# Performance work log

Hardware: AMD Instinct MI355X
Metric: run time of the kernel (lower is better)

Reference implementation:

```python
import jax, jax.numpy as jnp
import numpy as np

N = 100000   # nodes
E = 1200000  # edges
G = 512      # graphs in batch
H = 64       # hidden_dim
EED = 8      # edge_emb_dim
VOCABS = (120, 10, 7, 5, 2)
EDIMS = (64, 16, 8, 8, 4)
BN_EPS = 1e-5


def _lin(x, w, b):
    # torch nn.Linear: y = x @ W^T + b
    return x @ w.T + b


def setup_inputs() -> dict:
    key = jax.random.key(0)
    ks = iter(jax.random.split(key, 64))
    s = 0.02
    d = {}
    d["x"] = jax.random.randint(next(ks), (N, 5), 0, 120)
    d["edge_index"] = jax.random.randint(next(ks), (2, E), 0, N)
    d["edge_attr"] = jax.random.randint(next(ks), (E, 3), 0, 16)
    d["batch"] = jnp.sort(jax.random.randint(next(ks), (N,), 0, G))
    for i, (v, dd) in enumerate(zip(VOCABS, EDIMS)):
        d[f"emb{i}"] = jax.random.normal(next(ks), (v, dd), jnp.float32) * s
    d["proj_w"] = jax.random.normal(next(ks), (H, sum(EDIMS)), jnp.float32) * s
    d["proj_b"] = jnp.zeros((H,), jnp.float32)
    for i in (1, 2, 3):
        d[f"eemb{i}"] = jax.random.normal(next(ks), (16, EED), jnp.float32) * s
        d[f"lin_e{i}_w"] = jax.random.normal(next(ks), (H, EED), jnp.float32) * s
        d[f"lin_e{i}_b"] = jnp.zeros((H,), jnp.float32)
        d[f"eps{i}"] = jnp.zeros((), jnp.float32)
        d[f"mlp{i}_w1"] = jax.random.normal(next(ks), (H, H), jnp.float32) * s
        d[f"mlp{i}_b1"] = jnp.zeros((H,), jnp.float32)
        d[f"mlp{i}_w2"] = jax.random.normal(next(ks), (H, H), jnp.float32) * s
        d[f"mlp{i}_b2"] = jnp.zeros((H,), jnp.float32)
    d["bn_g"] = jnp.ones((H,), jnp.float32)
    d["bn_b"] = jnp.zeros((H,), jnp.float32)
    d["bn_rm"] = jnp.zeros((H,), jnp.float32)
    d["bn_rv"] = jnp.ones((H,), jnp.float32)
    d["gate_w"] = jax.random.normal(next(ks), (1, H), jnp.float32) * s
    d["gate_b"] = jnp.zeros((1,), jnp.float32)
    d["head_w1"] = jax.random.normal(next(ks), (128, H), jnp.float32) * s
    d["head_b1"] = jnp.zeros((128,), jnp.float32)
    d["head_w2"] = jax.random.normal(next(ks), (1, 128), jnp.float32) * s
    d["head_b2"] = jnp.zeros((1,), jnp.float32)
    return d


def reference(x, edge_index, edge_attr, batch,
              emb0, emb1, emb2, emb3, emb4, proj_w, proj_b,
              eemb1, lin_e1_w, lin_e1_b, eps1, mlp1_w1, mlp1_b1, mlp1_w2, mlp1_b2,
              eemb2, lin_e2_w, lin_e2_b, eps2, mlp2_w1, mlp2_b1, mlp2_w2, mlp2_b2,
              eemb3, lin_e3_w, lin_e3_b, eps3, mlp3_w1, mlp3_b1, mlp3_w2, mlp3_b2,
              bn_g, bn_b, bn_rm, bn_rv, gate_w, gate_b,
              head_w1, head_b1, head_w2, head_b2):
    # --- node embedding lookup (clamped per-table, as in torch) ---
    tabs = [emb0, emb1, emb2, emb3, emb4]
    feats = [t[jnp.clip(x[:, i], 0, t.shape[0] - 1)] for i, t in enumerate(tabs)]
    h = jnp.concatenate(feats, axis=-1)            # [N, 100]
    h = _lin(h, proj_w, proj_b)                    # [N, H]  (dropout = identity, eval)

    # --- edge hash, shared by all blocks ---
    eh = (edge_attr[:, 0] + 3 * edge_attr[:, 1] + 7 * edge_attr[:, 2]) % 16  # [E]
    src, dst = edge_index[0], edge_index[1]

    def gine(h, eemb, lw, lb, eps, w1, b1, w2, b2):
        # GINEConv: mlp((1+eps) x_i + sum_j relu(x_j + lin(e_ij)))
        e = _lin(eemb[eh], lw, lb)                        # [E, H]
        msg = jax.nn.relu(h[src] + e)                     # [E, H] gather + combine
        agg = jax.ops.segment_sum(msg, dst, num_segments=N)  # scatter-add to targets
        z = (1.0 + eps) * h + agg
        return _lin(jax.nn.relu(_lin(z, w1, b1)), w2, b2)

    h = jax.nn.relu(gine(h, eemb1, lin_e1_w, lin_e1_b, eps1, mlp1_w1, mlp1_b1, mlp1_w2, mlp1_b2))
    h = jax.nn.relu(gine(h, eemb2, lin_e2_w, lin_e2_b, eps2, mlp2_w1, mlp2_b1, mlp2_w2, mlp2_b2))
    h = jax.nn.relu(gine(h, eemb3, lin_e3_w, lin_e3_b, eps3, mlp3_w1, mlp3_b1, mlp3_w2, mlp3_b2))

    # BatchNorm1d (eval mode, running stats)
    h = (h - bn_rm) * jax.lax.rsqrt(bn_rv + BN_EPS) * bn_g + bn_b

    # AttentionalAggregation: segment softmax over gate, weighted segment sum
    gate = _lin(h, gate_w, gate_b)[:, 0]                  # [N]
    m = jax.ops.segment_max(gate, batch, num_segments=G)  # [G]
    w = jnp.exp(gate - m[batch])
    den = jax.ops.segment_sum(w, batch, num_segments=G) + 1e-16
    alpha = w / den[batch]                                # [N]
    graph = jax.ops.segment_sum(alpha[:, None] * h, batch, num_segments=G)  # [G, H]

    out = _lin(jax.nn.relu(_lin(graph, head_w1, head_b1)), head_w2, head_b2)  # [G, 1]
    return out[:, 0]
```

## Files before the change

kernel.cpp:

```cpp
#include <hip/hip_runtime.h>
#include <stdint.h>

#define N_NODES 100000
#define N_EDGES 1200000
#define N_GRAPH 512
#define HID 64

#define NBUCK 391
#define BCAP  4096
#define CHUNK 4096

#define PRE_W0  (144 * 64 + 3 * 1024 + 64 + NBUCK)
#define PRE_JOBS (PRE_W0 + 6 * 4096)

typedef __attribute__((ext_vector_type(8))) short bshort8;
typedef __attribute__((ext_vector_type(4))) float f32x4;

__device__ __forceinline__ unsigned short f2bf(float f) {
    unsigned u = __float_as_uint(f);
    u += 0x7FFF + ((u >> 16) & 1);
    return (unsigned short)(u >> 16);
}
__device__ __forceinline__ float bf2f(unsigned short b) {
    return __uint_as_float((unsigned)b << 16);
}

__global__ __launch_bounds__(256) void k_pre(
    const float* emb0, const float* emb1, const float* emb2, const float* emb3, const float* emb4,
    const float* proj_w,
    const float* ee1, const float* lw1, const float* lb1,
    const float* ee2, const float* lw2, const float* lb2,
    const float* ee3, const float* lw3, const float* lb3,
    const float* bn_g, const float* bn_b, const float* bn_rm, const float* bn_rv,
    const float* w11, const float* w12, const float* w21, const float* w22,
    const float* w31, const float* w32,
    float* ptab, float* elin, float* bnsc, float* bnsh, int* cursor,
    unsigned short* wbf)
{
    int job = blockIdx.x * 256 + threadIdx.x;
    if (job < 144 * 64) {
        int row = job >> 6, c = job & 63;
        const float* emb; int lr, dim, off;
        if (row < 120)      { emb = emb0; lr = row;       dim = 64; off = 0;  }
        else if (row < 130) { emb = emb1; lr = row - 120; dim = 16; off = 64; }
        else if (row < 137) { emb = emb2; lr = row - 130; dim = 8;  off = 80; }
        else if (row < 142) { emb = emb3; lr = row - 137; dim = 8;  off = 88; }
        else                { emb = emb4; lr = row - 142; dim = 4;  off = 96; }
        float s = 0.f;
        for (int d = 0; d < dim; ++d)
            s += emb[lr * dim + d] * proj_w[c * 100 + off + d];
        ptab[row * 64 + c] = s;
    } else if (job < 144 * 64 + 3 * 1024) {
        int j = job - 144 * 64;
        int L = j >> 10; int r = (j >> 6) & 15; int c = j & 63;
        const float* ee = (L == 0) ? ee1 : (L == 1) ? ee2 : ee3;
        const float* lw = (L == 0) ? lw1 : (L == 1) ? lw2 : lw3;
        const float* lb = (L == 0) ? lb1 : (L == 1) ? lb2 : lb3;
        float s = lb[c];
        for (int d = 0; d < 8; ++d) s += ee[r * 8 + d] * lw[c * 8 + d];
        elin[j] = s;
    } else if (job < 144 * 64 + 3 * 1024 + 64) {
        int c = job - (144 * 64 + 3 * 1024);
        float sc = bn_g[c] * rsqrtf(bn_rv[c] + 1e-5f);
        bnsc[c] = sc;
        bnsh[c] = bn_b[c] - bn_rm[c] * sc;
    } else if (job < PRE_W0) {
        cursor[job - (144 * 64 + 3 * 1024 + 64)] = 0;
    } else if (job < PRE_JOBS) {
        int j2 = job - PRE_W0;
        int sel = j2 >> 12;
        const float* W = (sel == 0) ? w11 : (sel == 1) ? w12 : (sel == 2) ? w21
                       : (sel == 3) ? w22 : (sel == 4) ? w31 : w32;
        wbf[j2] = f2bf(W[j2 & 4095]);
    }
}

__global__ __launch_bounds__(256) void k_embed(const int* x, const float* ptab,
                                               const float* proj_b, float* h,
                                               unsigned short* h2) {
    int id = blockIdx.x * 256 + threadIdx.x;
    if (id >= N_NODES * HID) return;
    int n = id >> 6, c = id & 63;
    const int* xr = x + n * 5;
    int r0 = min(max(xr[0], 0), 119);
    int r1 = 120 + min(max(xr[1], 0), 9);
    int r2 = 130 + min(max(xr[2], 0), 6);
    int r3 = 137 + min(max(xr[3], 0), 4);
    int r4 = 142 + min(max(xr[4], 0), 1);
    float v = proj_b[c] + ptab[r0 * 64 + c] + ptab[r1 * 64 + c] + ptab[r2 * 64 + c]
            + ptab[r3 * 64 + c] + ptab[r4 * 64 + c];
    h[id] = v;
    h2[id] = f2bf(v);
}

__global__ __launch_bounds__(256) void k_gptr(const int* batch, int* gptr) {
    int n = blockIdx.x * 256 + threadIdx.x;
    if (n >= N_NODES) return;
    int b = batch[n];
    int bp = (n == 0) ? -1 : batch[n - 1];
    for (int g = bp + 1; g <= b; ++g) gptr[g] = n;
    if (n == N_NODES - 1) {
        for (int g = b + 1; g <= N_GRAPH; ++g) gptr[g] = N_NODES;
    }
}

__global__ __launch_bounds__(256) void k_bin(const int* __restrict__ ei,
                                             const int* __restrict__ ea,
                                             int* __restrict__ cursor,
                                             int* __restrict__ binned) {
    __shared__ int pay[CHUNK];
    __shared__ unsigned short bkid[CHUNK];
    __shared__ int hist[NBUCK], inc[NBUCK], tmp[NBUCK], gdelta[NBUCK];
    int t = threadIdx.x;
    int e0 = blockIdx.x * CHUNK;
    for (int i = t; i < NBUCK; i += 256) hist[i] = 0;
    __syncthreads();
    int mypay[16], myrb[16];
    #pragma unroll
    for (int j = 0; j < 16; ++j) {
        int e = e0 + j * 256 + t;
        myrb[j] = -1;
        if (e < N_EDGES) {
            int s = ei[e];
            int d = ei[N_EDGES + e];
            int hsh = (ea[e * 3] + 3 * ea[e * 3 + 1] + 7 * ea[e * 3 + 2]) & 15;
            int b = d >> 8;
            mypay[j] = s | (hsh << 17) | ((d & 255) << 21);
            int r = atomicAdd(&hist[b], 1);
            myrb[j] = r | (b << 12);
        }
    }
    __syncthreads();
    for (int i = t; i < NBUCK; i += 256) inc[i] = hist[i];
    __syncthreads();
    for (int off = 1; off < NBUCK; off <<= 1) {
        for (int i = t; i < NBUCK; i += 256) tmp[i] = inc[i] + ((i >= off) ? inc[i - off] : 0);
        __syncthreads();
        for (int i = t; i < NBUCK; i += 256) inc[i] = tmp[i];
        __syncthreads();
    }
    for (int i = t; i < NBUCK; i += 256) {
        int c = hist[i];
        int gp = c ? atomicAdd(&cursor[i], c) : 0;
        gdelta[i] = i * BCAP + gp - (inc[i] - c);
    }
    __syncthreads();
    #pragma unroll
    for (int j = 0; j < 16; ++j) {
        if (myrb[j] >= 0) {
            int b = myrb[j] >> 12, r = myrb[j] & 0xFFF;
            int slot = (inc[b] - hist[b]) + r;
            pay[slot] = mypay[j];
            bkid[slot] = (unsigned short)b;
        }
    }
    __syncthreads();
    int tot = inc[NBUCK - 1];
    for (int i = t; i < tot; i += 256)
        binned[gdelta[bkid[i]] + i] = pay[i];
}

__global__ __launch_bounds__(512) void k_bscan(const int* cursor, int* bbase, int* rowptr) {
    __shared__ int s[512], tp[512];
    int t = threadIdx.x;
    int v = (t < NBUCK) ? cursor[t] : 0;
    s[t] = v;
    __syncthreads();
    for (int off = 1; off < 512; off <<= 1) {
        tp[t] = s[t] + ((t >= off) ? s[t - off] : 0);
        __syncthreads();
        s[t] = tp[t];
        __syncthreads();
    }
    if (t < NBUCK) bbase[t] = s[t] - v;
    if (t == 0) { bbase[NBUCK] = N_EDGES; rowptr[N_NODES] = N_EDGES; }
}

__global__ __launch_bounds__(256) void k_fin(const int* __restrict__ binned,
                                             const int* __restrict__ cursor,
                                             const int* __restrict__ bbase,
                                             int* __restrict__ rowptr,
                                             int* __restrict__ epk) {
    __shared__ int h2[256], sc[256], cur[256];
    int b = blockIdx.x, t = threadIdx.x;
    int cnt = cursor[b];
    int gb = bbase[b];
    int node0 = b << 8;
    h2[t] = 0;
    __syncthreads();
    const int* bp = binned + b * BCAP;
    for (int i = t; i < cnt; i += 256) atomicAdd(&h2[(bp[i] >> 21) & 255], 1);
    __syncthreads();
    sc[t] = h2[t];
    __syncthreads();
    for (int off = 1; off < 256; off <<= 1) {
        int v = (t >= off) ? sc[t - off] : 0;
        __syncthreads();
        sc[t] += v;
        __syncthreads();
    }
    int ex = sc[t] - h2[t];
    cur[t] = ex;
    int n = node0 + t;
    if (n < N_NODES) rowptr[n] = gb + ex;
    __syncthreads();
    for (int i = t; i < cnt; i += 256) {
        int p = bp[i];
        int pos = atomicAdd(&cur[(p >> 21) & 255], 1);
        epk[gb + pos] = p & 0x1FFFFF;
    }
}

__global__ __launch_bounds__(256) void k_gather(const unsigned short* __restrict__ h2,
                                                const float* __restrict__ elinL,
                                                const int* __restrict__ rowptr,
                                                const int* __restrict__ epk,
                                                float* __restrict__ agg) {
    __shared__ float es[16 * 64];
    int t = threadIdx.x;
    ((float4*)es)[t] = ((const float4*)elinL)[t];
    __syncthreads();
    int n = blockIdx.x * 4 + (t >> 6);
    if (n >= N_NODES) return;
    int lane = t & 63;
    int grp = lane >> 4;
    int c4 = (lane & 15) << 2;
    int p0 = rowptr[n], p1 = rowptr[n + 1];
    float4 acc = make_float4(0.f, 0.f, 0.f, 0.f);
    int p = p0 + grp;
    while (p + 4 < p1) {
        int pk0 = epk[p];
        int pk1 = epk[p + 4];
        ushort4 a0 = *(const ushort4*)(h2 + (pk0 & 0x1FFFF) * 64 + c4);
        ushort4 a1 = *(const ushort4*)(h2 + (pk1 & 0x1FFFF) * 64 + c4);
        float4 e0 = *(const float4*)(es + ((pk0 >> 17) & 15) * 64 + c4);
        float4 e1 = *(const float4*)(es + ((pk1 >> 17) & 15) * 64 + c4);
        acc.x += fmaxf(bf2f(a0.x) + e0.x, 0.f) + fmaxf(bf2f(a1.x) + e1.x, 0.f);
        acc.y += fmaxf(bf2f(a0.y) + e0.y, 0.f) + fmaxf(bf2f(a1.y) + e1.y, 0.f);
        acc.z += fmaxf(bf2f(a0.z) + e0.z, 0.f) + fmaxf(bf2f(a1.z) + e1.z, 0.f);
        acc.w += fmaxf(bf2f(a0.w) + e0.w, 0.f) + fmaxf(bf2f(a1.w) + e1.w, 0.f);
        p += 8;
    }
    if (p < p1) {
        int pk0 = epk[p];
        ushort4 a0 = *(const ushort4*)(h2 + (pk0 & 0x1FFFF) * 64 + c4);
        float4 e0 = *(const float4*)(es + ((pk0 >> 17) & 15) * 64 + c4);
        acc.x += fmaxf(bf2f(a0.x) + e0.x, 0.f);
        acc.y += fmaxf(bf2f(a0.y) + e0.y, 0.f);
        acc.z += fmaxf(bf2f(a0.z) + e0.z, 0.f);
        acc.w += fmaxf(bf2f(a0.w) + e0.w, 0.f);
    }
    acc.x += __shfl_down(acc.x, 32, 64);
    acc.y += __shfl_down(acc.y, 32, 64);
    acc.z += __shfl_down(acc.z, 32, 64);
    acc.w += __shfl_down(acc.w, 32, 64);
    acc.x += __shfl_down(acc.x, 16, 64);
    acc.y += __shfl_down(acc.y, 16, 64);
    acc.z += __shfl_down(acc.z, 16, 64);
    acc.w += __shfl_down(acc.w, 16, 64);
    if (grp == 0) *(float4*)(agg + n * 64 + c4) = acc;
}

__global__ __launch_bounds__(256) void k_mlpm(const float* __restrict__ hin,
                                              const float* __restrict__ agg,
                                              const float* __restrict__ epsp,
                                              const unsigned short* __restrict__ wbf1,
                                              const float* __restrict__ b1,
                                              const unsigned short* __restrict__ wbf2,
                                              const float* __restrict__ b2,
                                              float* __restrict__ out,
                                              unsigned short* __restrict__ h2out,
                                              const float* __restrict__ bnsc,
                                              const float* __restrict__ bnsh,
                                              const float* __restrict__ gate_w,
                                              const float* __restrict__ gate_b,
                                              float* __restrict__ gate) {
    __shared__ unsigned short zb[64 * 72];
    __shared__ unsigned short hb[64 * 72];
    int t = threadIdx.x;
    int row0 = blockIdx.x * 64;
    float epsv = 1.f + epsp[0];
    for (int idx = t; idx < 1024; idx += 256) {
        int r = idx >> 4, c4 = (idx & 15) << 2;
        int gr = row0 + r;
        float4 v = make_float4(0.f, 0.f, 0.f, 0.f);
        if (gr < N_NODES) {
            float4 a = *(const float4*)(hin + gr * 64 + c4);
            float4 b = *(const float4*)(agg + gr * 64 + c4);
            v.x = epsv * a.x + b.x; v.y = epsv * a.y + b.y;
            v.z = epsv * a.z + b.z; v.w = epsv * a.w + b.w;
        }
        ushort4 zv;
        zv.x = f2bf(v.x); zv.y = f2bf(v.y); zv.z = f2bf(v.z); zv.w = f2bf(v.w);
        *(ushort4*)(zb + r * 72 + c4) = zv;
    }
    int lane = t & 63, wv = t >> 6;
    int quad = lane >> 4, lc = lane & 15;
    int m0 = wv * 16;
    bshort8 w1f[4][2];
    #pragma unroll
    for (int nt = 0; nt < 4; ++nt)
        #pragma unroll
        for (int kt = 0; kt < 2; ++kt)
            w1f[nt][kt] = *(const bshort8*)(wbf1 + (nt * 16 + lc) * 64 + kt * 32 + quad * 8);
    bshort8 w2f[4][2];
    #pragma unroll
    for (int nt = 0; nt < 4; ++nt)
        #pragma unroll
        for (int kt = 0; kt < 2; ++kt)
            w2f[nt][kt] = *(const bshort8*)(wbf2 + (nt * 16 + lc) * 64 + kt * 32 + quad * 8);
    __syncthreads();
    bshort8 a0 = *(const bshort8*)(zb + (m0 + lc) * 72 + quad * 8);
    bshort8 a1 = *(const bshort8*)(zb + (m0 + lc) * 72 + 32 + quad * 8);
    f32x4 acc1[4];
    #pragma unroll
    for (int nt = 0; nt < 4; ++nt) {
        acc1[nt] = (f32x4){0.f, 0.f, 0.f, 0.f};
        acc1[nt] = __builtin_amdgcn_mfma_f32_16x16x32_bf16(a0, w1f[nt][0], acc1[nt], 0, 0, 0);
        acc1[nt] = __builtin_amdgcn_mfma_f32_16x16x32_bf16(a1, w1f[nt][1], acc1[nt], 0, 0, 0);
    }
    #pragma unroll
    for (int nt = 0; nt < 4; ++nt) {
        float bb = b1[nt * 16 + lc];
        #pragma unroll
        for (int reg = 0; reg < 4; ++reg) {
            float v = fmaxf(acc1[nt][reg] + bb, 0.f);
            hb[(m0 + quad * 4 + reg) * 72 + nt * 16 + lc] = f2bf(v);
        }
    }
    bshort8 c0 = *(const bshort8*)(hb + (m0 + lc) * 72 + quad * 8);
    bshort8 c1 = *(const bshort8*)(hb + (m0 + lc) * 72 + 32 + quad * 8);
    f32x4 acc2[4];
    #pragma unroll
    for (int nt = 0; nt < 4; ++nt) {
        acc2[nt] = (f32x4){0.f, 0.f, 0.f, 0.f};
        acc2[nt] = __builtin_amdgcn_mfma_f32_16x16x32_bf16(c0, w2f[nt][0], acc2[nt], 0, 0, 0);
        acc2[nt] = __builtin_amdgcn_mfma_f32_16x16x32_bf16(c1, w2f[nt][1], acc2[nt], 0, 0, 0);
    }
    if (gate == nullptr) {
        #pragma unroll
        for (int reg = 0; reg < 4; ++reg) {
            int gr = row0 + m0 + quad * 4 + reg;
            if (gr < N_NODES) {
                #pragma unroll
                for (int nt = 0; nt < 4; ++nt) {
                    int col = nt * 16 + lc;
                    float v = fmaxf(acc2[nt][reg] + b2[col], 0.f);
                    out[gr * 64 + col] = v;
                    h2out[gr * 64 + col] = f2bf(v);
                }
            }
        }
    } else {
        float gb = gate_b[0];
        #pragma unroll
        for (int reg = 0; reg < 4; ++reg) {
            int gr = row0 + m0 + quad * 4 + reg;
            float p = 0.f;
            #pragma unroll
            for (int nt = 0; nt < 4; ++nt) {
                int col = nt * 16 + lc;
                float v = fmaxf(acc2[nt][reg] + b2[col], 0.f) * bnsc[col] + bnsh[col];
                p += v * gate_w[col];
                if (gr < N_NODES) out[gr * 64 + col] = v;
            }
            p += __shfl_down(p, 8, 16);
            p += __shfl_down(p, 4, 16);
            p += __shfl_down(p, 2, 16);
            p += __shfl_down(p, 1, 16);
            if (lc == 0 && gr < N_NODES) gate[gr] = p + gb;
        }
    }
}

__global__ __launch_bounds__(256) void k_att(const float* __restrict__ h,
                                             const float* __restrict__ gate,
                                             const int* __restrict__ gptr,
                                             const float* __restrict__ hw1,
                                             const float* __restrict__ hb1,
                                             const float* __restrict__ hw2,
                                             const float* __restrict__ hb2,
                                             float* __restrict__ out) {
    __shared__ float red[4];
    __shared__ float acc_s[4][64];
    __shared__ float gvec[64];
    __shared__ float m_s, den_s;
    int t = threadIdx.x, g = blockIdx.x;
    int n0 = gptr[g], n1 = gptr[g + 1];
    float m = -INFINITY;
    for (int n = n0 + t; n < n1; n += 256) m = fmaxf(m, gate[n]);
    #pragma unroll
    for (int off = 32; off > 0; off >>= 1) m = fmaxf(m, __shfl_down(m, off, 64));
    if ((t & 63) == 0) red[t >> 6] = m;
    __syncthreads();
    if (t == 0) m_s = fmaxf(fmaxf(red[0], red[1]), fmaxf(red[2], red[3]));
    __syncthreads();
    m = m_s;
    float s = 0.f;
    for (int n = n0 + t; n < n1; n += 256) s += expf(gate[n] - m);
    #pragma unroll
    for (int off = 32; off > 0; off >>= 1) s += __shfl_down(s, off, 64);
    if ((t & 63) == 0) red[t >> 6] = s;
    __syncthreads();
    if (t == 0) den_s = red[0] + red[1] + red[2] + red[3] + 1e-16f;
    __syncthreads();
    float invden = 1.f / den_s;
    int c = t & 63, w = t >> 6;
    float acc = 0.f;
    for (int n = n0 + w; n < n1; n += 4) {
        float a = expf(gate[n] - m);
        acc += a * h[n * 64 + c];
    }
    acc_s[w][c] = acc;
    __syncthreads();
    if (w == 0)
        gvec[c] = (acc_s[0][c] + acc_s[1][c] + acc_s[2][c] + acc_s[3][c]) * invden;
    __syncthreads();
    float p = 0.f;
    if (t < 128) {
        float sh = hb1[t];
        const float* wr = hw1 + t * 64;
        #pragma unroll
        for (int k = 0; k < 64; ++k) sh += gvec[k] * wr[k];
        p = fmaxf(sh, 0.f) * hw2[t];
    }
    #pragma unroll
    for (int off = 32; off > 0; off >>= 1) p += __shfl_down(p, off, 64);
    if (t == 0) red[0] = p;
    if (t == 64) red[1] = p;
    __syncthreads();
    if (t == 0) out[g] = red[0] + red[1] + hb2[0];
}

extern "C" void kernel_launch(void* const* d_in, const int* in_sizes, int n_in,
                              void* d_out, int out_size, void* d_ws, size_t ws_size,
                              hipStream_t stream) {
    const int* x    = (const int*)d_in[0];
    const int* ei   = (const int*)d_in[1];
    const int* ea   = (const int*)d_in[2];
    const int* bat  = (const int*)d_in[3];
    const float* emb0 = (const float*)d_in[4];
    const float* emb1 = (const float*)d_in[5];
    const float* emb2 = (const float*)d_in[6];
    const float* emb3 = (const float*)d_in[7];
    const float* emb4 = (const float*)d_in[8];
    const float* proj_w = (const float*)d_in[9];
    const float* proj_b = (const float*)d_in[10];
    const float* bn_g  = (const float*)d_in[35];
    const float* bn_b  = (const float*)d_in[36];
    const float* bn_rm = (const float*)d_in[37];
    const float* bn_rv = (const float*)d_in[38];
    const float* gate_w = (const float*)d_in[39];
    const float* gate_b = (const float*)d_in[40];
    const float* head_w1 = (const float*)d_in[41];
    const float* head_b1 = (const float*)d_in[42];
    const float* head_w2 = (const float*)d_in[43];
    const float* head_b2 = (const float*)d_in[44];

    char* wsb = (char*)d_ws;
    size_t o = 0;
    auto alloc = [&](size_t bytes) -> void* {
        void* p = wsb + o;
        o += (bytes + 255) & ~(size_t)255;
        return p;
    };
    float* ptab   = (float*)alloc(144 * 64 * 4);
    float* elin   = (float*)alloc(3 * 16 * 64 * 4);
    float* bnsc   = (float*)alloc(64 * 4);
    float* bnsh   = (float*)alloc(64 * 4);
    int* cursor   = (int*)alloc(NBUCK * 4);
    int* bbase    = (int*)alloc((NBUCK + 1) * 4);
    int* gptr     = (int*)alloc((N_GRAPH + 1) * 4);
    int* rowptr   = (int*)alloc(((size_t)N_NODES + 1) * 4);
    int* binned   = (int*)alloc((size_t)NBUCK * BCAP * 4);
    int* epk      = (int*)alloc((size_t)N_EDGES * 4);
    float* h      = (float*)alloc((size_t)N_NODES * 64 * 4);
    unsigned short* h2 = (unsigned short*)alloc((size_t)N_NODES * 64 * 2);
    float* agg    = (float*)alloc((size_t)N_NODES * 64 * 4);
    float* gate   = (float*)alloc((size_t)N_NODES * 4);
    unsigned short* wbf = (unsigned short*)alloc(6 * 4096 * 2);

    k_pre<<<(PRE_JOBS + 255) / 256, 256, 0, stream>>>(
                                  emb0, emb1, emb2, emb3, emb4, proj_w,
                                  (const float*)d_in[11], (const float*)d_in[12], (const float*)d_in[13],
                                  (const float*)d_in[19], (const float*)d_in[20], (const float*)d_in[21],
                                  (const float*)d_in[27], (const float*)d_in[28], (const float*)d_in[29],
                                  bn_g, bn_b, bn_rm, bn_rv,
                                  (const float*)d_in[15], (const float*)d_in[17],
                                  (const float*)d_in[23], (const float*)d_in[25],
                                  (const float*)d_in[31], (const float*)d_in[33],
                                  ptab, elin, bnsc, bnsh, cursor, wbf);
    k_embed<<<(N_NODES * 64 + 255) / 256, 256, 0, stream>>>(x, ptab, proj_b, h, h2);
    k_gptr<<<(N_NODES + 255) / 256, 256, 0, stream>>>(bat, gptr);
    k_bin<<<(N_EDGES + CHUNK - 1) / CHUNK, 256, 0, stream>>>(ei, ea, cursor, binned);
    k_bscan<<<1, 512, 0, stream>>>(cursor, bbase, rowptr);
    k_fin<<<NBUCK, 256, 0, stream>>>(binned, cursor, bbase, rowptr, epk);

    for (int L = 0; L < 3; ++L) {
        const float* epsp = (const float*)d_in[14 + L * 8];
        const float* b1   = (const float*)d_in[16 + L * 8];
        const float* b2   = (const float*)d_in[18 + L * 8];
        const unsigned short* wb1 = wbf + (L * 2 + 0) * 4096;
        const unsigned short* wb2 = wbf + (L * 2 + 1) * 4096;
        k_gather<<<(N_NODES + 3) / 4, 256, 0, stream>>>(h2, elin + L * 1024, rowptr, epk, agg);
        if (L < 2) {
            k_mlpm<<<(N_NODES + 63) / 64, 256, 0, stream>>>(h, agg, epsp, wb1, b1, wb2, b2, h, h2,
                                                            nullptr, nullptr, nullptr, nullptr,
                                                            nullptr);
        } else {
            k_mlpm<<<(N_NODES + 63) / 64, 256, 0, stream>>>(h, agg, epsp, wb1, b1, wb2, b2, h, nullptr,
                                                            bnsc, bnsh, gate_w, gate_b, gate);
        }
    }

    k_att<<<N_GRAPH, 256, 0, stream>>>(h, gate, gptr, head_w1, head_b1, head_w2, head_b2,
                                       (float*)d_out);
}
```

Measured before the change: 445.3 us.

## Drop fp32 node features, keep bf16 only; preload edge indices via shuffle

Removes the fp32 copy of node features h throughout. Embed, MLP and attention kernels now read and write only the bf16 buffer, which cuts global memory traffic for the per-layer residual and the final pooling. Separately, the gather kernel loads up to 64 packed edge indices per node with one coalesced load and broadcasts them with wave shuffles instead of issuing per-edge global index loads. The trade-off is that the residual term and the pooled features lose precision by being rounded to bf16, and the MLP kernel reads and writes h2 in place.

```diff
diff --git a/kernel.cpp b/kernel.cpp
--- a/kernel.cpp
+++ b/kernel.cpp
@@ -76,8 +76,7 @@
 }
 
 __global__ __launch_bounds__(256) void k_embed(const int* x, const float* ptab,
-                                               const float* proj_b, float* h,
-                                               unsigned short* h2) {
+                                               const float* proj_b, unsigned short* h2) {
     int id = blockIdx.x * 256 + threadIdx.x;
     if (id >= N_NODES * HID) return;
     int n = id >> 6, c = id & 63;
@@ -89,7 +88,6 @@
     int r4 = 142 + min(max(xr[4], 0), 1);
     float v = proj_b[c] + ptab[r0 * 64 + c] + ptab[r1 * 64 + c] + ptab[r2 * 64 + c]
             + ptab[r3 * 64 + c] + ptab[r4 * 64 + c];
-    h[id] = v;
     h2[id] = f2bf(v);
 }
 
@@ -226,29 +224,40 @@
     int grp = lane >> 4;
     int c4 = (lane & 15) << 2;
     int p0 = rowptr[n], p1 = rowptr[n + 1];
+    int deg = p1 - p0;
+    int nb = min(deg, 64);
+    int pkv = (lane < deg) ? epk[p0 + lane] : 0;
     float4 acc = make_float4(0.f, 0.f, 0.f, 0.f);
-    int p = p0 + grp;
-    while (p + 4 < p1) {
-        int pk0 = epk[p];
-        int pk1 = epk[p + 4];
-        ushort4 a0 = *(const ushort4*)(h2 + (pk0 & 0x1FFFF) * 64 + c4);
-        ushort4 a1 = *(const ushort4*)(h2 + (pk1 & 0x1FFFF) * 64 + c4);
-        float4 e0 = *(const float4*)(es + ((pk0 >> 17) & 15) * 64 + c4);
-        float4 e1 = *(const float4*)(es + ((pk1 >> 17) & 15) * 64 + c4);
-        acc.x += fmaxf(bf2f(a0.x) + e0.x, 0.f) + fmaxf(bf2f(a1.x) + e1.x, 0.f);
-        acc.y += fmaxf(bf2f(a0.y) + e0.y, 0.f) + fmaxf(bf2f(a1.y) + e1.y, 0.f);
-        acc.z += fmaxf(bf2f(a0.z) + e0.z, 0.f) + fmaxf(bf2f(a1.z) + e1.z, 0.f);
-        acc.w += fmaxf(bf2f(a0.w) + e0.w, 0.f) + fmaxf(bf2f(a1.w) + e1.w, 0.f);
-        p += 8;
-    }
-    if (p < p1) {
-        int pk0 = epk[p];
-        ushort4 a0 = *(const ushort4*)(h2 + (pk0 & 0x1FFFF) * 64 + c4);
-        float4 e0 = *(const float4*)(es + ((pk0 >> 17) & 15) * 64 + c4);
-        acc.x += fmaxf(bf2f(a0.x) + e0.x, 0.f);
-        acc.y += fmaxf(bf2f(a0.y) + e0.y, 0.f);
-        acc.z += fmaxf(bf2f(a0.z) + e0.z, 0.f);
-        acc.w += fmaxf(bf2f(a0.w) + e0.w, 0.f);
+    #pragma unroll
+    for (int j = 0; j < 8; ++j) {
+        int e = grp + j * 4;
+        if (e < nb) {
+            int pk = __shfl(pkv, e, 64);
+            ushort4 a = *(const ushort4*)(h2 + (pk & 0x1FFFF) * 64 + c4);
+            float4 ev = *(const float4*)(es + ((pk >> 17) & 15) * 64 + c4);
+            acc.x += fmaxf(bf2f(a.x) + ev.x, 0.f);
+            acc.y += fmaxf(bf2f(a.y) + ev.y, 0.f);
+            acc.z += fmaxf(bf2f(a.z) + ev.z, 0.f);
+            acc.w += fmaxf(bf2f(a.w) + ev.w, 0.f);
+        }
+    }
+    for (int e = grp + 32; e < nb; e += 4) {
+        int pk = __shfl(pkv, e, 64);
+        ushort4 a = *(const ushort4*)(h2 + (pk & 0x1FFFF) * 64 + c4);
+        float4 ev = *(const float4*)(es + ((pk >> 17) & 15) * 64 + c4);
+        acc.x += fmaxf(bf2f(a.x) + ev.x, 0.f);
+        acc.y += fmaxf(bf2f(a.y) + ev.y, 0.f);
+        acc.z += fmaxf(bf2f(a.z) + ev.z, 0.f);
+        acc.w += fmaxf(bf2f(a.w) + ev.w, 0.f);
+    }
+    for (int p = p0 + 64 + grp; p < p1; p += 4) {
+        int pk = epk[p];
+        ushort4 a = *(const ushort4*)(h2 + (pk & 0x1FFFF) * 64 + c4);
+        float4 ev = *(const float4*)(es + ((pk >> 17) & 15) * 64 + c4);
+        acc.x += fmaxf(bf2f(a.x) + ev.x, 0.f);
+        acc.y += fmaxf(bf2f(a.y) + ev.y, 0.f);
+        acc.z += fmaxf(bf2f(a.z) + ev.z, 0.f);
+        acc.w += fmaxf(bf2f(a.w) + ev.w, 0.f);
     }
     acc.x += __shfl_down(acc.x, 32, 64);
     acc.y += __shfl_down(acc.y, 32, 64);
@@ -261,14 +270,13 @@
     if (grp == 0) *(float4*)(agg + n * 64 + c4) = acc;
 }
 
-__global__ __launch_bounds__(256) void k_mlpm(const float* __restrict__ hin,
+__global__ __launch_bounds__(256) void k_mlpm(const unsigned short* __restrict__ h2in,
                                               const float* __restrict__ agg,
                                               const float* __restrict__ epsp,
                                               const unsigned short* __restrict__ wbf1,
                                               const float* __restrict__ b1,
                                               const unsigned short* __restrict__ wbf2,
                                               const float* __restrict__ b2,
-                                              float* __restrict__ out,
                                               unsigned short* __restrict__ h2out,
                                               const float* __restrict__ bnsc,
                                               const float* __restrict__ bnsh,
@@ -283,15 +291,15 @@
     for (int idx = t; idx < 1024; idx += 256) {
         int r = idx >> 4, c4 = (idx & 15) << 2;
         int gr = row0 + r;
-        float4 v = make_float4(0.f, 0.f, 0.f, 0.f);
+        ushort4 zv = {0, 0, 0, 0};
         if (gr < N_NODES) {
-            float4 a = *(const float4*)(hin + gr * 64 + c4);
+            ushort4 a = *(const ushort4*)(h2in + gr * 64 + c4);
             float4 b = *(const float4*)(agg + gr * 64 + c4);
-            v.x = epsv * a.x + b.x; v.y = epsv * a.y + b.y;
-            v.z = epsv * a.z + b.z; v.w = epsv * a.w + b.w;
-        }
-        ushort4 zv;
-        zv.x = f2bf(v.x); zv.y = f2bf(v.y); zv.z = f2bf(v.z); zv.w = f2bf(v.w);
+            zv.x = f2bf(epsv * bf2f(a.x) + b.x);
+            zv.y = f2bf(epsv * bf2f(a.y) + b.y);
+            zv.z = f2bf(epsv * bf2f(a.z) + b.z);
+            zv.w = f2bf(epsv * bf2f(a.w) + b.w);
+        }
         *(ushort4*)(zb + r * 72 + c4) = zv;
     }
     int lane = t & 63, wv = t >> 6;
@@ -346,7 +354,6 @@
                 for (int nt = 0; nt < 4; ++nt) {
                     int col = nt * 16 + lc;
                     float v = fmaxf(acc2[nt][reg] + b2[col], 0.f);
-                    out[gr * 64 + col] = v;
                     h2out[gr * 64 + col] = f2bf(v);
                 }
             }
@@ -362,7 +369,7 @@
                 int col = nt * 16 + lc;
                 float v = fmaxf(acc2[nt][reg] + b2[col], 0.f) * bnsc[col] + bnsh[col];
                 p += v * gate_w[col];
-                if (gr < N_NODES) out[gr * 64 + col] = v;
+                if (gr < N_NODES) h2out[gr * 64 + col] = f2bf(v);
             }
             p += __shfl_down(p, 8, 16);
             p += __shfl_down(p, 4, 16);
@@ -373,7 +380,7 @@
     }
 }
 
-__global__ __launch_bounds__(256) void k_att(const float* __restrict__ h,
+__global__ __launch_bounds__(256) void k_att(const unsigned short* __restrict__ h2,
                                              const float* __restrict__ gate,
                                              const int* __restrict__ gptr,
                                              const float* __restrict__ hw1,
@@ -409,7 +416,7 @@
     float acc = 0.f;
     for (int n = n0 + w; n < n1; n += 4) {
         float a = expf(gate[n] - m);
-        acc += a * h[n * 64 + c];
+        acc += a * bf2f(h2[n * 64 + c]);
     }
     acc_s[w][c] = acc;
     __syncthreads();
@@ -474,7 +481,6 @@
     int* rowptr   = (int*)alloc(((size_t)N_NODES + 1) * 4);
     int* binned   = (int*)alloc((size_t)NBUCK * BCAP * 4);
     int* epk      = (int*)alloc((size_t)N_EDGES * 4);
-    float* h      = (float*)alloc((size_t)N_NODES * 64 * 4);
     unsigned short* h2 = (unsigned short*)alloc((size_t)N_NODES * 64 * 2);
     float* agg    = (float*)alloc((size_t)N_NODES * 64 * 4);
     float* gate   = (float*)alloc((size_t)N_NODES * 4);
@@ -490,7 +496,7 @@
                                   (const float*)d_in[23], (const float*)d_in[25],
                                   (const float*)d_in[31], (const float*)d_in[33],
                                   ptab, elin, bnsc, bnsh, cursor, wbf);
-    k_embed<<<(N_NODES * 64 + 255) / 256, 256, 0, stream>>>(x, ptab, proj_b, h, h2);
+    k_embed<<<(N_NODES * 64 + 255) / 256, 256, 0, stream>>>(x, ptab, proj_b, h2);
     k_gptr<<<(N_NODES + 255) / 256, 256, 0, stream>>>(bat, gptr);
     k_bin<<<(N_EDGES + CHUNK - 1) / CHUNK, 256, 0, stream>>>(ei, ea, cursor, binned);
     k_bscan<<<1, 512, 0, stream>>>(cursor, bbase, rowptr);
@@ -504,15 +510,15 @@
         const unsigned short* wb2 = wbf + (L * 2 + 1) * 4096;
         k_gather<<<(N_NODES + 3) / 4, 256, 0, stream>>>(h2, elin + L * 1024, rowptr, epk, agg);
         if (L < 2) {
-            k_mlpm<<<(N_NODES + 63) / 64, 256, 0, stream>>>(h, agg, epsp, wb1, b1, wb2, b2, h, h2,
+            k_mlpm<<<(N_NODES + 63) / 64, 256, 0, stream>>>(h2, agg, epsp, wb1, b1, wb2, b2, h2,
                                                             nullptr, nullptr, nullptr, nullptr,
                                                             nullptr);
         } else {
-            k_mlpm<<<(N_NODES + 63) / 64, 256, 0, stream>>>(h, agg, epsp, wb1, b1, wb2, b2, h, nullptr,
+            k_mlpm<<<(N_NODES + 63) / 64, 256, 0, stream>>>(h2, agg, epsp, wb1, b1, wb2, b2, h2,
                                                             bnsc, bnsh, gate_w, gate_b, gate);
         }
     }
 
-    k_att<<<N_GRAPH, 256, 0, stream>>>(h, gate, gptr, head_w1, head_b1, head_w2, head_b2,
+    k_att<<<N_GRAPH, 256, 0, stream>>>(h2, gate, gptr, head_w1, head_b1, head_w2, head_b2,
                                        (float*)d_out);
 }
```

Result: no change. 439.3 us (-1.4%).
